# Kernel optimization log

Hardware: AMD Instinct MI355X
Metric: run time of the kernel (lower is better)

The kernel has to match this reference:

```python
import jax, jax.numpy as jnp
import numpy as np

K_SIZE = 5
PAD = 2  # (dilation*(k-1)+1 - stride + 1)//2 with k=5, dilation=1, stride=1
DEPTH_MAX = 192.0
SAMPLE_NUM = 15


def setup_inputs() -> dict:
    key = jax.random.key(0)
    k1, k2, k3, k4 = jax.random.split(key, 4)
    b, c, h, w = 2, 32, 256, 512
    depth = jax.random.uniform(k1, (b, 1, h, w), jnp.float32) * 100.0
    features = jax.random.normal(k2, (b, c, h, w), jnp.float32)
    guide_weight = jax.random.uniform(k3, (b, h, w, K_SIZE * K_SIZE), jnp.float32)
    sample_idx = jax.random.randint(k4, (SAMPLE_NUM,), 0, K_SIZE * K_SIZE, dtype=jnp.int32)
    return {"depth": depth, "features": features, "guide_weight": guide_weight,
            "sample_idx": sample_idx}


def _gather(xpad, rows, cols):
    # xpad [b,c,H+2p,W+2p]; rows [s,h], cols [s,w] -> [b,c,s,h,w]
    return xpad[:, :, rows[:, :, None], cols[:, None, :]]


def reference(depth, features, guide_weight, sample_idx):
    b, c, h, w = features.shape
    d = depth.reshape(b, h, w)
    valid = ((d > 0) & (d < DEPTH_MAX)).astype(features.dtype)[:, None]  # [b,1,h,w]

    # Gaussian positional weights of the sampled kernel offsets (select_index)
    ctr = K_SIZE // 2
    px = (sample_idx % K_SIZE).astype(jnp.float32)
    py = (sample_idx // K_SIZE).astype(jnp.float32)
    dis = jnp.sqrt((px - ctr) ** 2 + (py - ctr) ** 2)
    pos_w = jnp.exp(-0.5 * dis)
    pos_w = pos_w / jnp.sum(pos_w)  # [s]

    # Direct gather at sampled kernel offsets (equivalent to unfold + index_select).
    # torch Unfold kernel-position ordering is row-major: p -> (ky=p//K, kx=p%K).
    dy = sample_idx // K_SIZE
    dx = sample_idx % K_SIZE
    rows = dy[:, None] + jnp.arange(h)[None, :]  # [s,h] indices into padded image
    cols = dx[:, None] + jnp.arange(w)[None, :]  # [s,w]

    fpad = jnp.pad(features, ((0, 0), (0, 0), (PAD, PAD), (PAD, PAD)))
    vpad = jnp.pad(valid, ((0, 0), (0, 0), (PAD, PAD), (PAD, PAD)))

    sampled = _gather(fpad, rows, cols)            # [b,c,s,h,w]
    valid_s = _gather(vpad, rows, cols)[:, 0]      # [b,s,h,w]
    guide_s = jnp.take(guide_weight, sample_idx, axis=3)    # [b,h,w,s]
    guide_s = jnp.transpose(guide_s, (0, 3, 1, 2))          # [b,s,h,w]

    wgt = valid_s * pos_w[None, :, None, None] * guide_s    # use_position & use_guide
    wgt = jax.nn.softmax(wgt, axis=1)
    out = jnp.einsum('bcshw,bshw->bchw', sampled, wgt)
    return (out, features)
```

## Files before the change

kernel.cpp:

```cpp
#include <hip/hip_runtime.h>
#include <math.h>

#define K_SIZE 5
#define PAD 2
#define DEPTH_MAX 192.0f
#define S_NUM 15
#define G_NUM (K_SIZE * K_SIZE)

#define B_DIM 2
#define C_DIM 32
#define H_DIM 256
#define W_DIM 512
#define HW (H_DIM * W_DIM)
#define NPX (B_DIM * HW)
#define CSPLIT 4
#define C_PER (C_DIM / CSPLIT)

__global__ __launch_bounds__(256) void weights_kernel(
    const float* __restrict__ depth,
    const float* __restrict__ guide,
    const int*   __restrict__ sample_idx,
    float*       __restrict__ w)
{
    __shared__ float gsh[4 * 64 * G_NUM];

    const int tid  = threadIdx.x;
    const int lane = tid & 63;
    const int wid  = tid >> 6;
    const int p    = blockIdx.x * 256 + tid;
    const int x = p % W_DIM;
    const int y = (p / W_DIM) % H_DIM;
    const int b = p / HW;

    int sidx[S_NUM];
#pragma unroll
    for (int s = 0; s < S_NUM; ++s) sidx[s] = sample_idx[s];

    {
        const int pw = blockIdx.x * 256 + (wid << 6);
        const float* gsrc = guide + (size_t)pw * G_NUM;
        float* gw = &gsh[wid * 64 * G_NUM];
#pragma unroll
        for (int k = 0; k < G_NUM; ++k)
            gw[lane + 64 * k] = gsrc[lane + 64 * k];
    }
    const float* grow = &gsh[wid * 64 * G_NUM + lane * G_NUM];

    float posw[S_NUM];
    float psum = 0.f;
#pragma unroll
    for (int s = 0; s < S_NUM; ++s) {
        const float px = (float)(sidx[s] % K_SIZE);
        const float py = (float)(sidx[s] / K_SIZE);
        const float ddx = px - (float)(K_SIZE / 2);
        const float ddy = py - (float)(K_SIZE / 2);
        posw[s] = expf(-0.5f * sqrtf(ddx * ddx + ddy * ddy));
        psum += posw[s];
    }
    const float inv_psum = 1.f / psum;

    float raw[S_NUM];
    float inb_f[S_NUM];
    const int dbase = b * HW;
#pragma unroll
    for (int s = 0; s < S_NUM; ++s) {
        const int dy = sidx[s] / K_SIZE - PAD;
        const int dx = sidx[s] % K_SIZE - PAD;
        const int yy = y + dy;
        const int xx = x + dx;
        const bool inb = (yy >= 0) & (yy < H_DIM) & (xx >= 0) & (xx < W_DIM);
        float v = 0.f;
        if (inb) {
            const float d = depth[dbase + yy * W_DIM + xx];
            v = (d > 0.f && d < DEPTH_MAX) ? 1.f : 0.f;
        }
        raw[s]   = v * (posw[s] * inv_psum) * grow[sidx[s]];
        inb_f[s] = inb ? 1.f : 0.f;
    }

    float mx = raw[0];
#pragma unroll
    for (int s = 1; s < S_NUM; ++s) mx = fmaxf(mx, raw[s]);
    float esum = 0.f;
    float wgt[S_NUM];
#pragma unroll
    for (int s = 0; s < S_NUM; ++s) {
        wgt[s] = expf(raw[s] - mx);
        esum += wgt[s];
    }
    const float inv_esum = 1.f / esum;

#pragma unroll
    for (int s = 0; s < S_NUM; ++s)
        w[s * NPX + p] = wgt[s] * inv_esum * inb_f[s];
}

__global__ __launch_bounds__(256) void gather_kernel(
    const float* __restrict__ features,
    const int*   __restrict__ sample_idx,
    const float* __restrict__ w,
    float*       __restrict__ out)
{
    const int p = blockIdx.x * 256 + threadIdx.x;
    const int x = p % W_DIM;
    const int y = (p / W_DIM) % H_DIM;
    const int b = p / HW;
    const int c0 = blockIdx.y * C_PER;

    int sidx[S_NUM];
#pragma unroll
    for (int s = 0; s < S_NUM; ++s) sidx[s] = sample_idx[s];

    float wgt[S_NUM];
#pragma unroll
    for (int s = 0; s < S_NUM; ++s) wgt[s] = w[s * NPX + p];

    int off[S_NUM];
#pragma unroll
    for (int s = 0; s < S_NUM; ++s) {
        const int dy = sidx[s] / K_SIZE - PAD;
        const int dx = sidx[s] % K_SIZE - PAD;
        const int yy = y + dy;
        const int xx = x + dx;
        const bool inb = (yy >= 0) & (yy < H_DIM) & (xx >= 0) & (xx < W_DIM);
        off[s] = inb ? (dy * W_DIM + dx) : 0;
    }

    const size_t hw   = (size_t)HW;
    const size_t feat = (size_t)B_DIM * C_DIM * hw;
    const size_t base = ((size_t)b * C_DIM + c0) * hw + (size_t)y * W_DIM + x;
    const float* fbase = features + base;
    float*       obase = out + base;
    float*       cbase = out + feat + base;
#pragma unroll 4
    for (int c = 0; c < C_PER; ++c) {
        const float ctr = fbase[0];
        float acc = 0.f;
#pragma unroll
        for (int s = 0; s < S_NUM; ++s) {
            acc = fmaf(fbase[off[s]], wgt[s], acc);
        }
        *obase = acc;
        *cbase = ctr;
        fbase += hw;
        obase += hw;
        cbase += hw;
    }
}

__global__ __launch_bounds__(256) void adaptive_sample_fused(
    const float* __restrict__ depth,
    const float* __restrict__ features,
    const float* __restrict__ guide,
    const int*   __restrict__ sample_idx,
    float*       __restrict__ out)
{
    __shared__ float gsh[4][64 * G_NUM];

    const int lane = threadIdx.x & 63;
    const int wid  = threadIdx.x >> 6;
    const int p = blockIdx.x * 256 + threadIdx.x;
    const int x = p % W_DIM;
    const int y = (p / W_DIM) % H_DIM;
    const int b = p / HW;
    const int c0 = blockIdx.y * C_PER;

    int sidx[S_NUM];
#pragma unroll
    for (int s = 0; s < S_NUM; ++s) sidx[s] = sample_idx[s];

    {
        const int pw = blockIdx.x * 256 + (wid << 6);
        const float* gsrc = guide + (size_t)pw * G_NUM;
        float* gw = gsh[wid];
#pragma unroll
        for (int k = 0; k < G_NUM; ++k)
            gw[lane + 64 * k] = gsrc[lane + 64 * k];
    }
    const float* grow = &gsh[wid][lane * G_NUM];

    float posw[S_NUM];
    float psum = 0.f;
#pragma unroll
    for (int s = 0; s < S_NUM; ++s) {
        const float px = (float)(sidx[s] % K_SIZE);
        const float py = (float)(sidx[s] / K_SIZE);
        const float ddx = px - (float)(K_SIZE / 2);
        const float ddy = py - (float)(K_SIZE / 2);
        posw[s] = expf(-0.5f * sqrtf(ddx * ddx + ddy * ddy));
        psum += posw[s];
    }
    const float inv_psum = 1.f / psum;

    float raw[S_NUM];
    int   off[S_NUM];
    float inb_f[S_NUM];
    const int dbase = b * HW;
#pragma unroll
    for (int s = 0; s < S_NUM; ++s) {
        const int dy = sidx[s] / K_SIZE - PAD;
        const int dx = sidx[s] % K_SIZE - PAD;
        const int yy = y + dy;
        const int xx = x + dx;
        const bool inb = (yy >= 0) & (yy < H_DIM) & (xx >= 0) & (xx < W_DIM);
        float v = 0.f;
        if (inb) {
            const float d = depth[dbase + yy * W_DIM + xx];
            v = (d > 0.f && d < DEPTH_MAX) ? 1.f : 0.f;
        }
        raw[s]   = v * (posw[s] * inv_psum) * grow[sidx[s]];
        off[s]   = inb ? (dy * W_DIM + dx) : 0;
        inb_f[s] = inb ? 1.f : 0.f;
    }

    float mx = raw[0];
#pragma unroll
    for (int s = 1; s < S_NUM; ++s) mx = fmaxf(mx, raw[s]);
    float esum = 0.f;
    float wgt[S_NUM];
#pragma unroll
    for (int s = 0; s < S_NUM; ++s) {
        wgt[s] = expf(raw[s] - mx);
        esum += wgt[s];
    }
    const float inv_esum = 1.f / esum;
#pragma unroll
    for (int s = 0; s < S_NUM; ++s)
        wgt[s] = wgt[s] * inv_esum * inb_f[s];

    const size_t hw   = (size_t)HW;
    const size_t feat = (size_t)B_DIM * C_DIM * hw;
    const size_t base = ((size_t)b * C_DIM + c0) * hw + (size_t)y * W_DIM + x;
    const float* fbase = features + base;
    float*       obase = out + base;
    float*       cbase = out + feat + base;
#pragma unroll 4
    for (int c = 0; c < C_PER; ++c) {
        const float ctr = fbase[0];
        float acc = 0.f;
#pragma unroll
        for (int s = 0; s < S_NUM; ++s) {
            acc = fmaf(fbase[off[s]], wgt[s], acc);
        }
        *obase = acc;
        *cbase = ctr;
        fbase += hw;
        obase += hw;
        cbase += hw;
    }
}

extern "C" void kernel_launch(void* const* d_in, const int* in_sizes, int n_in,
                              void* d_out, int out_size, void* d_ws, size_t ws_size,
                              hipStream_t stream) {
    const float* depth      = (const float*)d_in[0];
    const float* features   = (const float*)d_in[1];
    const float* guide      = (const float*)d_in[2];
    const int*   sample_idx = (const int*)d_in[3];

    float* out = (float*)d_out;
    const size_t ws_needed = (size_t)S_NUM * NPX * sizeof(float);

    const int blocks = NPX / 256;

    if (ws_size >= ws_needed && d_ws != nullptr) {
        float* w = (float*)d_ws;
        weights_kernel<<<blocks, 256, 0, stream>>>(depth, guide, sample_idx, w);
        dim3 grid(blocks, CSPLIT, 1);
        gather_kernel<<<grid, 256, 0, stream>>>(features, sample_idx, w, out);
    } else {
        dim3 grid(blocks, CSPLIT, 1);
        adaptive_sample_fused<<<grid, 256, 0, stream>>>(depth, features, guide,
                                                        sample_idx, out);
    }
}
```

Measured before the change: 154.4 us.

## Fuse weight computation and gather into one kernel covering all channels

Removes the two-kernel path that wrote softmax weights to workspace and read them back. A single kernel now computes the weights once per pixel and loops over all 32 channels instead of splitting channels across four grid slices. Output and copied-feature stores become nontemporal. This drops the workspace traffic and the redundant per-slice weight computation, but leaves 4x fewer blocks, each doing a longer serial channel loop.

```diff
diff --git a/kernel.cpp b/kernel.cpp
--- a/kernel.cpp
+++ b/kernel.cpp
@@ -13,142 +13,8 @@
 #define W_DIM 512
 #define HW (H_DIM * W_DIM)
 #define NPX (B_DIM * HW)
-#define CSPLIT 4
-#define C_PER (C_DIM / CSPLIT)
 
-__global__ __launch_bounds__(256) void weights_kernel(
-    const float* __restrict__ depth,
-    const float* __restrict__ guide,
-    const int*   __restrict__ sample_idx,
-    float*       __restrict__ w)
-{
-    __shared__ float gsh[4 * 64 * G_NUM];
-
-    const int tid  = threadIdx.x;
-    const int lane = tid & 63;
-    const int wid  = tid >> 6;
-    const int p    = blockIdx.x * 256 + tid;
-    const int x = p % W_DIM;
-    const int y = (p / W_DIM) % H_DIM;
-    const int b = p / HW;
-
-    int sidx[S_NUM];
-#pragma unroll
-    for (int s = 0; s < S_NUM; ++s) sidx[s] = sample_idx[s];
-
-    {
-        const int pw = blockIdx.x * 256 + (wid << 6);
-        const float* gsrc = guide + (size_t)pw * G_NUM;
-        float* gw = &gsh[wid * 64 * G_NUM];
-#pragma unroll
-        for (int k = 0; k < G_NUM; ++k)
-            gw[lane + 64 * k] = gsrc[lane + 64 * k];
-    }
-    const float* grow = &gsh[wid * 64 * G_NUM + lane * G_NUM];
-
-    float posw[S_NUM];
-    float psum = 0.f;
-#pragma unroll
-    for (int s = 0; s < S_NUM; ++s) {
-        const float px = (float)(sidx[s] % K_SIZE);
-        const float py = (float)(sidx[s] / K_SIZE);
-        const float ddx = px - (float)(K_SIZE / 2);
-        const float ddy = py - (float)(K_SIZE / 2);
-        posw[s] = expf(-0.5f * sqrtf(ddx * ddx + ddy * ddy));
-        psum += posw[s];
-    }
-    const float inv_psum = 1.f / psum;
-
-    float raw[S_NUM];
-    float inb_f[S_NUM];
-    const int dbase = b * HW;
-#pragma unroll
-    for (int s = 0; s < S_NUM; ++s) {
-        const int dy = sidx[s] / K_SIZE - PAD;
-        const int dx = sidx[s] % K_SIZE - PAD;
-        const int yy = y + dy;
-        const int xx = x + dx;
-        const bool inb = (yy >= 0) & (yy < H_DIM) & (xx >= 0) & (xx < W_DIM);
-        float v = 0.f;
-        if (inb) {
-            const float d = depth[dbase + yy * W_DIM + xx];
-            v = (d > 0.f && d < DEPTH_MAX) ? 1.f : 0.f;
-        }
-        raw[s]   = v * (posw[s] * inv_psum) * grow[sidx[s]];
-        inb_f[s] = inb ? 1.f : 0.f;
-    }
-
-    float mx = raw[0];
-#pragma unroll
-    for (int s = 1; s < S_NUM; ++s) mx = fmaxf(mx, raw[s]);
-    float esum = 0.f;
-    float wgt[S_NUM];
-#pragma unroll
-    for (int s = 0; s < S_NUM; ++s) {
-        wgt[s] = expf(raw[s] - mx);
-        esum += wgt[s];
-    }
-    const float inv_esum = 1.f / esum;
-
-#pragma unroll
-    for (int s = 0; s < S_NUM; ++s)
-        w[s * NPX + p] = wgt[s] * inv_esum * inb_f[s];
-}
-
-__global__ __launch_bounds__(256) void gather_kernel(
-    const float* __restrict__ features,
-    const int*   __restrict__ sample_idx,
-    const float* __restrict__ w,
-    float*       __restrict__ out)
-{
-    const int p = blockIdx.x * 256 + threadIdx.x;
-    const int x = p % W_DIM;
-    const int y = (p / W_DIM) % H_DIM;
-    const int b = p / HW;
-    const int c0 = blockIdx.y * C_PER;
-
-    int sidx[S_NUM];
-#pragma unroll
-    for (int s = 0; s < S_NUM; ++s) sidx[s] = sample_idx[s];
-
-    float wgt[S_NUM];
-#pragma unroll
-    for (int s = 0; s < S_NUM; ++s) wgt[s] = w[s * NPX + p];
-
-    int off[S_NUM];
-#pragma unroll
-    for (int s = 0; s < S_NUM; ++s) {
-        const int dy = sidx[s] / K_SIZE - PAD;
-        const int dx = sidx[s] % K_SIZE - PAD;
-        const int yy = y + dy;
-        const int xx = x + dx;
-        const bool inb = (yy >= 0) & (yy < H_DIM) & (xx >= 0) & (xx < W_DIM);
-        off[s] = inb ? (dy * W_DIM + dx) : 0;
-    }
-
-    const size_t hw   = (size_t)HW;
-    const size_t feat = (size_t)B_DIM * C_DIM * hw;
-    const size_t base = ((size_t)b * C_DIM + c0) * hw + (size_t)y * W_DIM + x;
-    const float* fbase = features + base;
-    float*       obase = out + base;
-    float*       cbase = out + feat + base;
-#pragma unroll 4
-    for (int c = 0; c < C_PER; ++c) {
-        const float ctr = fbase[0];
-        float acc = 0.f;
-#pragma unroll
-        for (int s = 0; s < S_NUM; ++s) {
-            acc = fmaf(fbase[off[s]], wgt[s], acc);
-        }
-        *obase = acc;
-        *cbase = ctr;
-        fbase += hw;
-        obase += hw;
-        cbase += hw;
-    }
-}
-
-__global__ __launch_bounds__(256) void adaptive_sample_fused(
+__global__ __launch_bounds__(256) void adaptive_sample_fused_all(
     const float* __restrict__ depth,
     const float* __restrict__ features,
     const float* __restrict__ guide,
@@ -163,7 +29,6 @@
     const int x = p % W_DIM;
     const int y = (p / W_DIM) % H_DIM;
     const int b = p / HW;
-    const int c0 = blockIdx.y * C_PER;
 
     int sidx[S_NUM];
 #pragma unroll
@@ -230,20 +95,20 @@
 
     const size_t hw   = (size_t)HW;
     const size_t feat = (size_t)B_DIM * C_DIM * hw;
-    const size_t base = ((size_t)b * C_DIM + c0) * hw + (size_t)y * W_DIM + x;
+    const size_t base = (size_t)b * C_DIM * hw + (size_t)y * W_DIM + x;
     const float* fbase = features + base;
     float*       obase = out + base;
     float*       cbase = out + feat + base;
 #pragma unroll 4
-    for (int c = 0; c < C_PER; ++c) {
+    for (int c = 0; c < C_DIM; ++c) {
         const float ctr = fbase[0];
         float acc = 0.f;
 #pragma unroll
         for (int s = 0; s < S_NUM; ++s) {
             acc = fmaf(fbase[off[s]], wgt[s], acc);
         }
-        *obase = acc;
-        *cbase = ctr;
+        __builtin_nontemporal_store(acc, obase);
+        __builtin_nontemporal_store(ctr, cbase);
         fbase += hw;
         obase += hw;
         cbase += hw;
@@ -259,18 +124,8 @@
     const int*   sample_idx = (const int*)d_in[3];
 
     float* out = (float*)d_out;
-    const size_t ws_needed = (size_t)S_NUM * NPX * sizeof(float);
-
     const int blocks = NPX / 256;
 
-    if (ws_size >= ws_needed && d_ws != nullptr) {
-        float* w = (float*)d_ws;
-        weights_kernel<<<blocks, 256, 0, stream>>>(depth, guide, sample_idx, w);
-        dim3 grid(blocks, CSPLIT, 1);
-        gather_kernel<<<grid, 256, 0, stream>>>(features, sample_idx, w, out);
-    } else {
-        dim3 grid(blocks, CSPLIT, 1);
-        adaptive_sample_fused<<<grid, 256, 0, stream>>>(depth, features, guide,
-                                                        sample_idx, out);
-    }
+    adaptive_sample_fused_all<<<blocks, 256, 0, stream>>>(depth, features, guide,
+                                                          sample_idx, out);
 }
```

New measurement: 202.7 us. 31.3% more time.

## Map channel groups to wavefronts within a block sharing pixel weights

Applied to the files above, without the earlier changes.

The gather kernel now assigns 64 pixels per block with each of four wavefronts handling a different 8-channel group, instead of splitting channels across grid.y. The fused fallback computes softmax weights once per pixel in one wavefront and shares them through LDS with a barrier, removing redundant depth/guide loads and softmax work across channel groups. The fallback trades three idle wavefronts during the weight phase and a block sync for less duplicated work.

```diff
diff --git a/kernel.cpp b/kernel.cpp
--- a/kernel.cpp
+++ b/kernel.cpp
@@ -13,8 +13,8 @@
 #define W_DIM 512
 #define HW (H_DIM * W_DIM)
 #define NPX (B_DIM * HW)
-#define CSPLIT 4
-#define C_PER (C_DIM / CSPLIT)
+#define PX_PER_BLK 64
+#define C_PER 8
 
 __global__ __launch_bounds__(256) void weights_kernel(
     const float* __restrict__ depth,
@@ -95,25 +95,27 @@
         w[s * NPX + p] = wgt[s] * inv_esum * inb_f[s];
 }
 
-__global__ __launch_bounds__(256) void gather_kernel(
+__global__ __launch_bounds__(256) void gather_kernel_v2(
     const float* __restrict__ features,
     const int*   __restrict__ sample_idx,
     const float* __restrict__ w,
     float*       __restrict__ out)
 {
-    const int p = blockIdx.x * 256 + threadIdx.x;
+    const int lane = threadIdx.x & 63;
+    const int wid  = threadIdx.x >> 6;
+    const int p = blockIdx.x * PX_PER_BLK + lane;
     const int x = p % W_DIM;
     const int y = (p / W_DIM) % H_DIM;
     const int b = p / HW;
-    const int c0 = blockIdx.y * C_PER;
+    const int c0 = wid * C_PER;
+
+    float wgt[S_NUM];
+#pragma unroll
+    for (int s = 0; s < S_NUM; ++s) wgt[s] = w[s * NPX + p];
 
     int sidx[S_NUM];
 #pragma unroll
     for (int s = 0; s < S_NUM; ++s) sidx[s] = sample_idx[s];
-
-    float wgt[S_NUM];
-#pragma unroll
-    for (int s = 0; s < S_NUM; ++s) wgt[s] = w[s * NPX + p];
 
     int off[S_NUM];
 #pragma unroll
@@ -148,54 +150,85 @@
     }
 }
 
-__global__ __launch_bounds__(256) void adaptive_sample_fused(
+__global__ __launch_bounds__(256) void adaptive_sample_fused_v3(
     const float* __restrict__ depth,
     const float* __restrict__ features,
     const float* __restrict__ guide,
     const int*   __restrict__ sample_idx,
     float*       __restrict__ out)
 {
-    __shared__ float gsh[4][64 * G_NUM];
+    __shared__ float gsh[PX_PER_BLK * G_NUM];
+    __shared__ float wsh[PX_PER_BLK * S_NUM];
 
     const int lane = threadIdx.x & 63;
     const int wid  = threadIdx.x >> 6;
-    const int p = blockIdx.x * 256 + threadIdx.x;
+    const int p = blockIdx.x * PX_PER_BLK + lane;
     const int x = p % W_DIM;
     const int y = (p / W_DIM) % H_DIM;
     const int b = p / HW;
-    const int c0 = blockIdx.y * C_PER;
+    const int c0 = wid * C_PER;
 
     int sidx[S_NUM];
 #pragma unroll
     for (int s = 0; s < S_NUM; ++s) sidx[s] = sample_idx[s];
 
-    {
-        const int pw = blockIdx.x * 256 + (wid << 6);
-        const float* gsrc = guide + (size_t)pw * G_NUM;
-        float* gw = gsh[wid];
+    if (wid == 0) {
+        const float* gsrc = guide + (size_t)blockIdx.x * PX_PER_BLK * G_NUM;
 #pragma unroll
         for (int k = 0; k < G_NUM; ++k)
-            gw[lane + 64 * k] = gsrc[lane + 64 * k];
-    }
-    const float* grow = &gsh[wid][lane * G_NUM];
-
-    float posw[S_NUM];
-    float psum = 0.f;
-#pragma unroll
-    for (int s = 0; s < S_NUM; ++s) {
-        const float px = (float)(sidx[s] % K_SIZE);
-        const float py = (float)(sidx[s] / K_SIZE);
-        const float ddx = px - (float)(K_SIZE / 2);
-        const float ddy = py - (float)(K_SIZE / 2);
-        posw[s] = expf(-0.5f * sqrtf(ddx * ddx + ddy * ddy));
-        psum += posw[s];
-    }
-    const float inv_psum = 1.f / psum;
-
-    float raw[S_NUM];
-    int   off[S_NUM];
-    float inb_f[S_NUM];
-    const int dbase = b * HW;
+            gsh[lane + 64 * k] = gsrc[lane + 64 * k];
+        const float* grow = &gsh[lane * G_NUM];
+
+        float posw[S_NUM];
+        float psum = 0.f;
+#pragma unroll
+        for (int s = 0; s < S_NUM; ++s) {
+            const float px = (float)(sidx[s] % K_SIZE);
+            const float py = (float)(sidx[s] / K_SIZE);
+            const float ddx = px - (float)(K_SIZE / 2);
+            const float ddy = py - (float)(K_SIZE / 2);
+            posw[s] = expf(-0.5f * sqrtf(ddx * ddx + ddy * ddy));
+            psum += posw[s];
+        }
+        const float inv_psum = 1.f / psum;
+
+        float raw[S_NUM];
+        float inb_f[S_NUM];
+        const int dbase = b * HW;
+#pragma unroll
+        for (int s = 0; s < S_NUM; ++s) {
+            const int dy = sidx[s] / K_SIZE - PAD;
+            const int dx = sidx[s] % K_SIZE - PAD;
+            const int yy = y + dy;
+            const int xx = x + dx;
+            const bool inb = (yy >= 0) & (yy < H_DIM) & (xx >= 0) & (xx < W_DIM);
+            float v = 0.f;
+            if (inb) {
+                const float d = depth[dbase + yy * W_DIM + xx];
+                v = (d > 0.f && d < DEPTH_MAX) ? 1.f : 0.f;
+            }
+            raw[s]   = v * (posw[s] * inv_psum) * grow[sidx[s]];
+            inb_f[s] = inb ? 1.f : 0.f;
+        }
+
+        float mx = raw[0];
+#pragma unroll
+        for (int s = 1; s < S_NUM; ++s) mx = fmaxf(mx, raw[s]);
+        float esum = 0.f;
+        float wgt[S_NUM];
+#pragma unroll
+        for (int s = 0; s < S_NUM; ++s) {
+            wgt[s] = expf(raw[s] - mx);
+            esum += wgt[s];
+        }
+        const float inv_esum = 1.f / esum;
+#pragma unroll
+        for (int s = 0; s < S_NUM; ++s)
+            wsh[lane * S_NUM + s] = wgt[s] * inv_esum * inb_f[s];
+    }
+    __syncthreads();
+
+    int off[S_NUM];
 #pragma unroll
     for (int s = 0; s < S_NUM; ++s) {
         const int dy = sidx[s] / K_SIZE - PAD;
@@ -203,30 +236,12 @@
         const int yy = y + dy;
         const int xx = x + dx;
         const bool inb = (yy >= 0) & (yy < H_DIM) & (xx >= 0) & (xx < W_DIM);
-        float v = 0.f;
-        if (inb) {
-            const float d = depth[dbase + yy * W_DIM + xx];
-            v = (d > 0.f && d < DEPTH_MAX) ? 1.f : 0.f;
-        }
-        raw[s]   = v * (posw[s] * inv_psum) * grow[sidx[s]];
-        off[s]   = inb ? (dy * W_DIM + dx) : 0;
-        inb_f[s] = inb ? 1.f : 0.f;
-    }
-
-    float mx = raw[0];
-#pragma unroll
-    for (int s = 1; s < S_NUM; ++s) mx = fmaxf(mx, raw[s]);
-    float esum = 0.f;
+        off[s] = inb ? (dy * W_DIM + dx) : 0;
+    }
+
     float wgt[S_NUM];
 #pragma unroll
-    for (int s = 0; s < S_NUM; ++s) {
-        wgt[s] = expf(raw[s] - mx);
-        esum += wgt[s];
-    }
-    const float inv_esum = 1.f / esum;
-#pragma unroll
-    for (int s = 0; s < S_NUM; ++s)
-        wgt[s] = wgt[s] * inv_esum * inb_f[s];
+    for (int s = 0; s < S_NUM; ++s) wgt[s] = wsh[lane * S_NUM + s];
 
     const size_t hw   = (size_t)HW;
     const size_t feat = (size_t)B_DIM * C_DIM * hw;
@@ -260,17 +275,14 @@
 
     float* out = (float*)d_out;
     const size_t ws_needed = (size_t)S_NUM * NPX * sizeof(float);
-
-    const int blocks = NPX / 256;
+    const int blocks = NPX / PX_PER_BLK;
 
     if (ws_size >= ws_needed && d_ws != nullptr) {
         float* w = (float*)d_ws;
-        weights_kernel<<<blocks, 256, 0, stream>>>(depth, guide, sample_idx, w);
-        dim3 grid(blocks, CSPLIT, 1);
-        gather_kernel<<<grid, 256, 0, stream>>>(features, sample_idx, w, out);
+        weights_kernel<<<NPX / 256, 256, 0, stream>>>(depth, guide, sample_idx, w);
+        gather_kernel_v2<<<blocks, 256, 0, stream>>>(features, sample_idx, w, out);
     } else {
-        dim3 grid(blocks, CSPLIT, 1);
-        adaptive_sample_fused<<<grid, 256, 0, stream>>>(depth, features, guide,
-                                                        sample_idx, out);
-    }
-}
+        adaptive_sample_fused_v3<<<blocks, 256, 0, stream>>>(depth, features, guide,
+                                                             sample_idx, out);
+    }
+}
```

New measurement: 161.1 us. +4.3%, slower.
